# Performance work log

Measured on AMD Instinct MI355X. Metric: run time of the kernel, lower is better.

The kernel has to match this reference:

```python
import jax, jax.numpy as jnp
import numpy as np

DIM = 1024
SEQ_LEN = 4096
K_RANK = 256
HEADS = 16
HEAD_DIM = DIM // HEADS
BATCH = 4


def setup_inputs() -> dict:
    key = jax.random.key(0)
    k1, k2, k3, k4 = jax.random.split(key, 4)
    x = jax.random.normal(k1, (BATCH, SEQ_LEN, DIM), dtype=jnp.float32)
    W_qkv = jax.random.normal(k2, (DIM, 3 * DIM), dtype=jnp.float32) * (DIM ** -0.5)
    E = jax.random.normal(k3, (SEQ_LEN, K_RANK), dtype=jnp.float32)
    W_out = jax.random.normal(k4, (DIM, DIM), dtype=jnp.float32) * (DIM ** -0.5)
    b_out = jnp.zeros((DIM,), dtype=jnp.float32)
    return {"x": x, "W_qkv": W_qkv, "E": E, "W_out": W_out, "b_out": b_out}


def reference(x, W_qkv, E, W_out, b_out):
    B, N, D = x.shape
    scale = HEAD_DIM ** -0.5
    qkv = x @ W_qkv                                    # [B, N, 3D]
    q, k, v = jnp.split(qkv, 3, axis=-1)
    # [B, N, D] -> [B, H, N, hd]
    reshape_heads = lambda t: t.reshape(B, N, HEADS, HEAD_DIM).transpose(0, 2, 1, 3)
    q, k, v = map(reshape_heads, (q, k, v))
    # Linformer low-rank projection along sequence: [B, H, N, hd] -> [B, H, k, hd]
    k_proj = jnp.einsum('bhnd,nk->bhkd', k, E)
    v_proj = jnp.einsum('bhnd,nk->bhkd', v, E)
    scores = jnp.einsum('bhnd,bhkd->bhnk', q, k_proj) * scale  # [B, H, N, k]
    attn = jax.nn.softmax(scores, axis=-1)
    out = jnp.einsum('bhnk,bhkd->bhnd', attn, v_proj)  # [B, H, N, hd]
    out = out.transpose(0, 2, 1, 3).reshape(B, N, D)
    return out @ W_out + b_out
```

## Files before the change

kernel.cpp:

```cpp
#include <hip/hip_runtime.h>
#include <hip/hip_bf16.h>

typedef _Float16 f16;
typedef __attribute__((ext_vector_type(4))) _Float16 f16x4;
typedef __attribute__((ext_vector_type(8))) _Float16 f16x8;
typedef __attribute__((ext_vector_type(4))) float f32x4;

#define DIM 1024
#define SEQ 4096
#define KRNK 256
#define NH 16
#define HD 64
#define NB 4
#define ROWS (NB*SEQ)
#define NSPLIT 4

typedef const void __attribute__((address_space(1))) as1cv;
typedef void __attribute__((address_space(3))) as3v;

static __device__ __forceinline__ void glds16(const void* g, void* l) {
  __builtin_amdgcn_global_load_lds((as1cv*)g, (as3v*)l, 16, 0, 0);
}

__global__ __launch_bounds__(256) void k_prep_w_all(const float* __restrict__ Wqkv,
                                                    const float* __restrict__ Wout,
                                                    f16* __restrict__ Wph,
                                                    f16* __restrict__ Wpl,
                                                    f16* __restrict__ WoT) {
  __shared__ float tile[64][65];
  int bx = blockIdx.x;
  const float* in; f16* oh; f16* ol; int C; bool split;
  if (bx < 768) { in = Wqkv; oh = Wph; ol = Wpl; C = 3 * DIM; split = true; }
  else { bx -= 768; in = Wout; oh = WoT; ol = nullptr; C = DIM; split = false; }
  const int R = DIM;
  int rtiles = R >> 6;
  int rt = bx % rtiles, ct = bx / rtiles;
  int r0 = rt << 6, c0 = ct << 6, t = threadIdx.x;
#pragma unroll
  for (int i = 0; i < 16; ++i) {
    int e = t + i * 256; int r = e >> 6, c = e & 63;
    tile[r][c] = in[(size_t)(r0 + r) * C + c0 + c];
  }
  __syncthreads();
#pragma unroll
  for (int i = 0; i < 16; ++i) {
    int e = t + i * 256; int c = e >> 6, r = e & 63;
    float v = tile[r][c];
    size_t idx = (size_t)(c0 + c) * R + r0 + r;
    if (split) {
      v *= 256.0f;
      f16 h = (f16)v;
      oh[idx] = h;
      ol[idx] = (f16)(v - (float)h);
    } else {
      oh[idx] = (f16)v;
    }
  }
}

template<bool WH>
__global__ __launch_bounds__(256) void k_tsplit(const float* __restrict__ in,
                                                f16* __restrict__ oh,
                                                f16* __restrict__ oth,
                                                int R, int C) {
  __shared__ __align__(16) f16 tileT[64][66];
  int rtiles = R >> 6;
  int rt = blockIdx.x % rtiles, ct = blockIdx.x / rtiles;
  int r0 = rt << 6, c0 = ct << 6, t = threadIdx.x;
  int cq = (t & 15) * 4, rr = t >> 4;
#pragma unroll
  for (int i = 0; i < 4; ++i) {
    int r = rr + i * 16;
    f32x4 v = *(const f32x4*)&in[(size_t)(r0 + r) * C + c0 + cq];
    f16x4 h4 = {(f16)v[0], (f16)v[1], (f16)v[2], (f16)v[3]};
    if constexpr (WH) *(f16x4*)&oh[(size_t)(r0 + r) * C + c0 + cq] = h4;
#pragma unroll
    for (int k = 0; k < 4; ++k) tileT[cq + k][r] = h4[k];
  }
  __syncthreads();
  {
    int c = t >> 2, seg = t & 3;
    f16x8 a = *(const f16x8*)&tileT[c][seg * 16];
    f16x8 b = *(const f16x8*)&tileT[c][seg * 16 + 8];
    f16* dst = &oth[(size_t)(c0 + c) * R + r0 + seg * 16];
    *(f16x8*)dst = a;
    *(f16x8*)(dst + 8) = b;
  }
}

template<bool ASPL, bool BSPL, int MT, int NT>
static __device__ __forceinline__ void mm_core(
    const f16* __restrict__ Ah, const f16* __restrict__ Al, int lda,
    const f16* __restrict__ Bh, const f16* __restrict__ Bl, int ldb,
    int bm, int bn, int K,
    f16* sAh, f16* sAl, f16* sBh, f16* sBl,
    f32x4 (&acc)[MT / 32][NT / 32]) {
  constexpr int MREP = MT / 32, NREP = NT / 32;
  constexpr int AI = MT / 32, BI = NT / 32;
  const int t = threadIdx.x;
  const int lane = t & 63, w = t >> 6;
  const int wr = w >> 1, wc = w & 1;
  const int l15 = lane & 15, hi = lane >> 4;
  const f32x4 zero = {0.f, 0.f, 0.f, 0.f};
#pragma unroll
  for (int m = 0; m < MREP; ++m)
#pragma unroll
    for (int n = 0; n < NREP; ++n) acc[m][n] = zero;

  for (int kk = 0; kk < K; kk += 64) {
#pragma unroll
    for (int i = 0; i < AI; ++i) {
      int c = t + i * 256;
      int row = c >> 3, cc = c & 7;
      size_t g = (size_t)(bm + row) * lda + kk + ((cc ^ (row & 7)) * 8);
      glds16(Ah + g, &sAh[c * 8]);
      if constexpr (ASPL) glds16(Al + g, &sAl[c * 8]);
    }
#pragma unroll
    for (int i = 0; i < BI; ++i) {
      int c = t + i * 256;
      int row = c >> 3, cc = c & 7;
      size_t g = (size_t)(bn + row) * ldb + kk + ((cc ^ (row & 7)) * 8);
      glds16(Bh + g, &sBh[c * 8]);
      if constexpr (BSPL) glds16(Bl + g, &sBl[c * 8]);
    }
    __syncthreads();

    f16x8 avh[MREP][2], avl[MREP][2], bvh[NREP][2], bvl[NREP][2];
#pragma unroll
    for (int m = 0; m < MREP; ++m)
#pragma unroll
      for (int ks = 0; ks < 2; ++ks) {
        int R = wr * (MT / 2) + m * 16 + l15;
        int off = R * 64 + (((ks * 4 + hi) ^ (R & 7)) * 8);
        avh[m][ks] = *(const f16x8*)&sAh[off];
        if constexpr (ASPL) avl[m][ks] = *(const f16x8*)&sAl[off];
      }
#pragma unroll
    for (int n = 0; n < NREP; ++n)
#pragma unroll
      for (int ks = 0; ks < 2; ++ks) {
        int R = wc * (NT / 2) + n * 16 + l15;
        int off = R * 64 + (((ks * 4 + hi) ^ (R & 7)) * 8);
        bvh[n][ks] = *(const f16x8*)&sBh[off];
        if constexpr (BSPL) bvl[n][ks] = *(const f16x8*)&sBl[off];
      }
#pragma unroll
    for (int m = 0; m < MREP; ++m)
#pragma unroll
      for (int n = 0; n < NREP; ++n)
#pragma unroll
        for (int ks = 0; ks < 2; ++ks) {
          if constexpr (ASPL && BSPL) {
            acc[m][n] = __builtin_amdgcn_mfma_f32_16x16x32_f16(avl[m][ks], bvh[n][ks], acc[m][n], 0, 0, 0);
            acc[m][n] = __builtin_amdgcn_mfma_f32_16x16x32_f16(avh[m][ks], bvl[n][ks], acc[m][n], 0, 0, 0);
          } else if constexpr (BSPL) {
            acc[m][n] = __builtin_amdgcn_mfma_f32_16x16x32_f16(avh[m][ks], bvl[n][ks], acc[m][n], 0, 0, 0);
          }
          acc[m][n] = __builtin_amdgcn_mfma_f32_16x16x32_f16(avh[m][ks], bvh[n][ks], acc[m][n], 0, 0, 0);
        }
    __syncthreads();
  }
}

__global__ __launch_bounds__(256) void k_xe2(const f16* __restrict__ Eth,
                                             const f16* __restrict__ xth,
                                             float* __restrict__ XEp) {
  __shared__ __align__(16) f16 sA[128 * 64];
  __shared__ __align__(16) f16 sB[64 * 64];
  int bx = blockIdx.x;
  int nt = bx & 15, mt = (bx >> 4) & 1, b = (bx >> 5) & 3, sp = bx >> 7;
  int bm = mt << 7, bn = nt << 6;
  int koff = sp * (SEQ / NSPLIT);
  f32x4 acc[4][2];
  mm_core<false, false, 128, 64>(Eth + koff, nullptr, SEQ,
                                 xth + (size_t)b * SEQ + koff, nullptr, ROWS,
                                 bm, bn, SEQ / NSPLIT, sA, nullptr, sB, nullptr, acc);
  const int t = threadIdx.x, lane = t & 63, w = t >> 6;
  const int wr = w >> 1, wc = w & 1, l15 = lane & 15, hi = lane >> 4;
#pragma unroll
  for (int m = 0; m < 4; ++m)
#pragma unroll
    for (int n = 0; n < 2; ++n)
#pragma unroll
      for (int r = 0; r < 4; ++r) {
        int kr = bm + wr * 64 + m * 16 + hi * 4 + r;
        int dd = bn + wc * 32 + n * 16 + l15;
        XEp[(((size_t)sp * NB + b) * KRNK + kr) * DIM + dd] = acc[m][n][r];
      }
}

__global__ __launch_bounds__(256) void k_xered(const float* __restrict__ XEp,
                                               f16* __restrict__ XEh) {
  size_t i = (size_t)blockIdx.x * 256 + threadIdx.x;
  const size_t sstride = (size_t)NB * KRNK * DIM / 4;
  const f32x4* p = (const f32x4*)XEp;
  f32x4 s = p[i];
#pragma unroll
  for (int sp = 1; sp < NSPLIT; ++sp) s += p[i + sp * sstride];
  f16x4 h4 = {(f16)s[0], (f16)s[1], (f16)s[2], (f16)s[3]};
  *(f16x4*)&XEh[i * 4] = h4;
}

__global__ __launch_bounds__(256) void k_gq(const f16* __restrict__ xh,
                                            const f16* __restrict__ Wph,
                                            f16* __restrict__ q) {
  __shared__ __align__(16) f16 sA[128 * 64];
  __shared__ __align__(16) f16 sB[128 * 64];
  int bx = blockIdx.x;
  int mt = bx & 127, nt = bx >> 7;
  int bm = mt << 7, bn = nt << 7;
  f32x4 acc[4][4];
  mm_core<false, false, 128, 128>(xh, nullptr, DIM, Wph, nullptr, DIM, bm, bn, DIM,
                                  sA, nullptr, sB, nullptr, acc);
  const int t = threadIdx.x, lane = t & 63, w = t >> 6;
  const int wr = w >> 1, wc = w & 1, l15 = lane & 15, hi = lane >> 4;
#pragma unroll
  for (int m = 0; m < 4; ++m)
#pragma unroll
    for (int n = 0; n < 4; ++n)
#pragma unroll
      for (int r = 0; r < 4; ++r) {
        int row = bm + wr * 64 + m * 16 + hi * 4 + r;
        int col = bn + wc * 64 + n * 16 + l15;
        q[(size_t)row * DIM + col] = (f16)(acc[m][n][r] * (1.0f / 256.0f));
      }
}

__global__ __launch_bounds__(256) void k_t2(const f16* __restrict__ XEh,
                                            const f16* __restrict__ Wph,
                                            const f16* __restrict__ Wpl,
                                            f16* __restrict__ kph,
                                            f16* __restrict__ vpt) {
  __shared__ __align__(16) f16 sAh[128 * 64];
  __shared__ __align__(16) f16 sBh[64 * 64], sBl[64 * 64];
  int bx = blockIdx.x;
  int nt = bx & 15, mt = (bx >> 4) & 1, b = (bx >> 5) & 3, kv = bx >> 7;
  size_t abase = (size_t)b * KRNK * DIM;
  size_t wbase = (size_t)(DIM + kv * DIM) * DIM;
  f32x4 acc[4][2];
  mm_core<false, true, 128, 64>(XEh + abase, nullptr, DIM, Wph + wbase, Wpl + wbase, DIM,
                                mt << 7, nt << 6, DIM, sAh, nullptr, sBh, sBl, acc);
  const int t = threadIdx.x, lane = t & 63, w = t >> 6;
  const int wr = w >> 1, wc = w & 1, l15 = lane & 15, hi = lane >> 4;
#pragma unroll
  for (int m = 0; m < 4; ++m)
#pragma unroll
    for (int n = 0; n < 2; ++n)
#pragma unroll
      for (int r = 0; r < 4; ++r) {
        int row = (mt << 7) + wr * 64 + m * 16 + hi * 4 + r;
        int col = (nt << 6) + wc * 32 + n * 16 + l15;
        float s = acc[m][n][r] * (1.0f / 256.0f);
        if (!kv) kph[((size_t)(b * KRNK + row)) * DIM + col] = (f16)s;
        else     vpt[((size_t)(b * DIM + col)) * KRNK + row] = (f16)s;
      }
}

__global__ __launch_bounds__(256) void k_attn(const f16* __restrict__ q,
                                              const f16* __restrict__ kph,
                                              const f16* __restrict__ vpt,
                                              f16* __restrict__ oattn) {
  __shared__ __align__(16) f16 sBuf[2][128 * 64];
  __shared__ __align__(16) f16 sP[64 * KRNK];
  int bx0 = blockIdx.x;
  int swz = (bx0 & 7) * 512 + (bx0 >> 3);
  int qb = swz & 63;
  int bh = swz >> 6;
  int b = bh >> 4, h = bh & 15;
  int t = threadIdx.x;
  int lane = t & 63, w = t >> 6;
  int l15 = lane & 15, hi = lane >> 4;

  const f16* kbase = kph + ((size_t)(b * KRNK)) * DIM + h * HD;
  const f16* vbase = vpt + ((size_t)(b * DIM + h * HD)) * KRNK;

  auto stageK = [&](int c, int bufi) {
#pragma unroll
    for (int i = 0; i < 4; ++i) {
      int c2 = t + i * 256;
      int kr = c2 >> 3, sl = c2 & 7;
      glds16(kbase + (size_t)(c * 128 + kr) * DIM + ((sl ^ (kr & 7)) * 8),
             &sBuf[bufi][c2 * 8]);
    }
  };
  auto stageV = [&](int c, int bufi) {
#pragma unroll
    for (int i = 0; i < 4; ++i) {
      int c2 = t + i * 256;
      int hd = c2 >> 4, sl = c2 & 15;
      glds16(vbase + (size_t)hd * KRNK + c * 128 + ((sl ^ (hd & 7)) * 8),
             &sBuf[bufi][c2 * 8]);
    }
  };

  int seqrow = qb * 64 + w * 16 + l15;
  const f16* qg = q + ((size_t)(b * SEQ + seqrow)) * DIM + h * HD;
  f16x8 aq[2];
  aq[0] = *(const f16x8*)(qg + hi * 8);
  aq[1] = *(const f16x8*)(qg + 32 + hi * 8);

  const f32x4 zero = {0.f, 0.f, 0.f, 0.f};
  f32x4 s[16];

  stageK(0, 0);
#pragma unroll
  for (int c = 0; c < 2; ++c) {
    __syncthreads();
    if (c == 0) stageK(1, 1);
    else        stageV(0, 0);
#pragma unroll
    for (int n = 0; n < 8; ++n) {
      int nn = c * 8 + n;
      s[nn] = zero;
      int krl = n * 16 + l15;
#pragma unroll
      for (int ks = 0; ks < 2; ++ks) {
        f16x8 bk = *(const f16x8*)&sBuf[c][krl * 64 + (((ks * 4 + hi) ^ (krl & 7)) * 8)];
        s[nn] = __builtin_amdgcn_mfma_f32_16x16x32_f16(bk, aq[ks], s[nn], 0, 0, 0);
      }
    }
  }

  const float scale = 0.125f;
  float m0 = s[0][0];
#pragma unroll
  for (int n = 0; n < 16; ++n)
#pragma unroll
    for (int r = 0; r < 4; ++r) m0 = fmaxf(m0, s[n][r]);
  m0 = fmaxf(m0, __shfl_xor(m0, 16));
  m0 = fmaxf(m0, __shfl_xor(m0, 32));
  float sm0 = 0.f, sm1 = 0.f, sm2 = 0.f, sm3 = 0.f;
#pragma unroll
  for (int n = 0; n < 16; ++n) {
    float p0 = __expf((s[n][0] - m0) * scale);
    float p1 = __expf((s[n][1] - m0) * scale);
    float p2 = __expf((s[n][2] - m0) * scale);
    float p3 = __expf((s[n][3] - m0) * scale);
    s[n][0] = p0; s[n][1] = p1; s[n][2] = p2; s[n][3] = p3;
    sm0 += p0; sm1 += p1; sm2 += p2; sm3 += p3;
  }
  float sm = (sm0 + sm1) + (sm2 + sm3);
  sm += __shfl_xor(sm, 16);
  sm += __shfl_xor(sm, 32);
  float inv = 1.0f / sm;

  {
    int qrow = w * 16 + l15;
    int qm = qrow & 7;
    f16* rowp = &sP[qrow * KRNK];
#pragma unroll
    for (int n = 0; n < 16; ++n) {
      int chunk = 2 * n + (hi >> 1);
      f16x4 pv = {(f16)s[n][0], (f16)s[n][1], (f16)s[n][2], (f16)s[n][3]};
      *(f16x4*)&rowp[((chunk ^ qm) * 8) + (hi & 1) * 4] = pv;
    }
  }

  f32x4 o[4];
#pragma unroll
  for (int n = 0; n < 4; ++n) o[n] = zero;
  int qloc = w * 16 + l15;
#pragma unroll
  for (int c = 0; c < 2; ++c) {
    __syncthreads();
    if (c == 0) stageV(1, 1);
#pragma unroll
    for (int q4 = 0; q4 < 4; ++q4) {
      int chunk = c * 16 + q4 * 4 + hi;
      f16x8 pa = *(const f16x8*)&sP[qloc * KRNK + ((chunk ^ (qloc & 7)) * 8)];
#pragma unroll
      for (int n = 0; n < 4; ++n) {
        int hd = n * 16 + l15;
        f16x8 bv = *(const f16x8*)&sBuf[c][hd * 128 + (((q4 * 4 + hi) ^ (hd & 7)) * 8)];
        o[n] = __builtin_amdgcn_mfma_f32_16x16x32_f16(pa, bv, o[n], 0, 0, 0);
      }
    }
  }

  float invr[4];
#pragma unroll
  for (int r = 0; r < 4; ++r) invr[r] = __shfl(inv, hi * 4 + r);

  size_t obase = ((size_t)(b * SEQ + qb * 64)) * DIM + h * HD;
#pragma unroll
  for (int n = 0; n < 4; ++n)
#pragma unroll
    for (int r = 0; r < 4; ++r) {
      int qloc2 = w * 16 + hi * 4 + r;
      int hd = n * 16 + l15;
      oattn[obase + (size_t)qloc2 * DIM + hd] = (f16)(o[n][r] * invr[r]);
    }
}

__global__ __launch_bounds__(256) void k_go(const f16* __restrict__ oattn,
                                            const f16* __restrict__ WoT,
                                            const float* __restrict__ bias,
                                            float* __restrict__ out) {
  __shared__ __align__(16) f16 sA[128 * 64];
  __shared__ __align__(16) f16 sB[128 * 64];
  int bx = blockIdx.x;
  int mt = bx & 127, nt = bx >> 7;
  int bm = mt << 7, bn = nt << 7;
  f32x4 acc[4][4];
  mm_core<false, false, 128, 128>(oattn, nullptr, DIM, WoT, nullptr, DIM, bm, bn, DIM,
                                  sA, nullptr, sB, nullptr, acc);
  const int t = threadIdx.x, lane = t & 63, w = t >> 6;
  const int wr = w >> 1, wc = w & 1, l15 = lane & 15, hi = lane >> 4;
#pragma unroll
  for (int m = 0; m < 4; ++m)
#pragma unroll
    for (int n = 0; n < 4; ++n)
#pragma unroll
      for (int r = 0; r < 4; ++r) {
        int row = bm + wr * 64 + m * 16 + hi * 4 + r;
        int col = bn + wc * 64 + n * 16 + l15;
        out[(size_t)row * DIM + col] = acc[m][n][r] + bias[col];
      }
}

extern "C" void kernel_launch(void* const* d_in, const int* in_sizes, int n_in,
                              void* d_out, int out_size, void* d_ws, size_t ws_size,
                              hipStream_t stream) {
  const float* x    = (const float*)d_in[0];
  const float* Wqkv = (const float*)d_in[1];
  const float* E    = (const float*)d_in[2];
  const float* Wout = (const float*)d_in[3];
  const float* bout = (const float*)d_in[4];
  float* out = (float*)d_out;

  char* p = (char*)d_ws;
  f16* Wph = (f16*)p;  p += (size_t)2 * 3 * DIM * DIM;
  f16* Wpl = (f16*)p;  p += (size_t)2 * 3 * DIM * DIM;
  f16* WoT = (f16*)p;  p += (size_t)2 * DIM * DIM;
  f16* xh  = (f16*)p;  p += (size_t)2 * ROWS * DIM;
  f16* xth = (f16*)p;  p += (size_t)2 * DIM * ROWS;
  f16* Eth = (f16*)p;  p += (size_t)2 * KRNK * SEQ;
  f16* XEh = (f16*)p;  p += (size_t)2 * NB * KRNK * DIM;
  f16* kph = (f16*)p;  p += (size_t)2 * NB * KRNK * DIM;
  f16* vpt = (f16*)p;  p += (size_t)2 * NB * DIM * KRNK;
  f16* oattn = (f16*)p; p += (size_t)2 * ROWS * DIM;
  float* XEp = (float*)p;  p += (size_t)4 * NSPLIT * NB * KRNK * DIM;
  size_t need = (size_t)(p - (char*)d_ws);
  if (ws_size < need) return;

  f16* q = xth;

  k_prep_w_all<<<1024, 256, 0, stream>>>(Wqkv, Wout, Wph, Wpl, WoT);
  k_tsplit<true><<<(ROWS / 64) * (DIM / 64), 256, 0, stream>>>(x, xh, xth, ROWS, DIM);
  k_tsplit<false><<<(SEQ / 64) * (KRNK / 64), 256, 0, stream>>>(E, nullptr, Eth, SEQ, KRNK);
  k_xe2<<<512, 256, 0, stream>>>(Eth, xth, XEp);
  k_xered<<<(NB * KRNK * DIM / 4) / 256, 256, 0, stream>>>(XEp, XEh);
  k_gq<<<1024, 256, 0, stream>>>(xh, Wph, q);
  k_t2<<<256, 256, 0, stream>>>(XEh, Wph, Wpl, kph, vpt);
  k_attn<<<64 * 64, 256, 0, stream>>>(q, kph, vpt, oattn);
  k_go<<<1024, 256, 0, stream>>>(oattn, WoT, bout, out);
}
```

Before: 223.8 us.

## Rewrite output projection GEMM as 256x256 double-buffered 8-wave kernel

Replaces the 128x128-tile output projection kernel with a 256x256-tile, 512-thread kernel. It double-buffers LDS, interleaves the async global-to-LDS loads for the next K tile with four MFMA phases of the current tile, and uses XOR-swizzled LDS addressing and setprio around the MFMA bursts. The goal is to raise data reuse and hide global load latency. In exchange it uses 128KB of LDS per block, and the 256-block grid may underfill the 256 CUs or limit occupancy.

```diff
diff --git a/kernel.cpp b/kernel.cpp
--- a/kernel.cpp
+++ b/kernel.cpp
@@ -393,27 +393,106 @@
     }
 }
 
-__global__ __launch_bounds__(256) void k_go(const f16* __restrict__ oattn,
-                                            const f16* __restrict__ WoT,
-                                            const float* __restrict__ bias,
-                                            float* __restrict__ out) {
-  __shared__ __align__(16) f16 sA[128 * 64];
-  __shared__ __align__(16) f16 sB[128 * 64];
-  int bx = blockIdx.x;
-  int mt = bx & 127, nt = bx >> 7;
-  int bm = mt << 7, bn = nt << 7;
-  f32x4 acc[4][4];
-  mm_core<false, false, 128, 128>(oattn, nullptr, DIM, WoT, nullptr, DIM, bm, bn, DIM,
-                                  sA, nullptr, sB, nullptr, acc);
-  const int t = threadIdx.x, lane = t & 63, w = t >> 6;
-  const int wr = w >> 1, wc = w & 1, l15 = lane & 15, hi = lane >> 4;
-#pragma unroll
-  for (int m = 0; m < 4; ++m)
+__global__ __launch_bounds__(512) void k_go8(const f16* __restrict__ oattn,
+                                             const f16* __restrict__ WoT,
+                                             const float* __restrict__ bias,
+                                             float* __restrict__ out) {
+  __shared__ __align__(16) f16 sA[2][256 * 64];
+  __shared__ __align__(16) f16 sB[2][256 * 64];
+  const int bx = blockIdx.x;
+  const int mt = bx & 63, nt = bx >> 6;
+  const int bm = mt << 8, bn = nt << 8;
+  const int t = threadIdx.x;
+  const int lane = t & 63, w = t >> 6;
+  const int wr = w >> 2, wc = w & 3;
+  const int l15 = lane & 15, hi = lane >> 4;
+  const f32x4 zero = {0.f, 0.f, 0.f, 0.f};
+  f32x4 acc[8][4];
+#pragma unroll
+  for (int m = 0; m < 8; ++m)
+#pragma unroll
+    for (int n = 0; n < 4; ++n) acc[m][n] = zero;
+
+  auto stage = [&](const f16* base, int boff, int kk, int half, f16* lds) {
+#pragma unroll
+    for (int i = 0; i < 2; ++i) {
+      int c = t + i * 512;
+      int row = c >> 3, sl = c & 7;
+      glds16(base + (size_t)(boff + half * 128 + row) * DIM + kk + ((sl ^ (row & 7)) * 8),
+             lds + half * 8192 + c * 8);
+    }
+  };
+
+  auto phase = [&](const f16* cA, const f16* cB, int qm, int qn) {
+    f16x8 av[4][2], bv[2][2];
+#pragma unroll
+    for (int mi = 0; mi < 4; ++mi)
+#pragma unroll
+      for (int ks = 0; ks < 2; ++ks) {
+        int R = wr * 128 + (qm * 4 + mi) * 16 + l15;
+        av[mi][ks] = *(const f16x8*)&cA[R * 64 + (((ks * 4 + hi) ^ (R & 7)) * 8)];
+      }
+#pragma unroll
+    for (int ni = 0; ni < 2; ++ni)
+#pragma unroll
+      for (int ks = 0; ks < 2; ++ks) {
+        int R = wc * 64 + (qn * 2 + ni) * 16 + l15;
+        bv[ni][ks] = *(const f16x8*)&cB[R * 64 + (((ks * 4 + hi) ^ (R & 7)) * 8)];
+      }
+    __builtin_amdgcn_s_setprio(1);
+#pragma unroll
+    for (int mi = 0; mi < 4; ++mi)
+#pragma unroll
+      for (int ni = 0; ni < 2; ++ni)
+#pragma unroll
+        for (int ks = 0; ks < 2; ++ks)
+          acc[qm * 4 + mi][qn * 2 + ni] =
+              __builtin_amdgcn_mfma_f32_16x16x32_f16(av[mi][ks], bv[ni][ks],
+                                                     acc[qm * 4 + mi][qn * 2 + ni], 0, 0, 0);
+    __builtin_amdgcn_s_setprio(0);
+  };
+
+  constexpr int NT_K = DIM / 64;
+  stage(oattn, bm, 0, 0, sA[0]);
+  stage(oattn, bm, 0, 1, sA[0]);
+  stage(WoT,   bn, 0, 0, sB[0]);
+  stage(WoT,   bn, 0, 1, sB[0]);
+
+  for (int ti = 0; ti < NT_K; ++ti) {
+    const int cur = ti & 1;
+    const f16* cA = sA[cur];
+    const f16* cB = sB[cur];
+    f16* nA = sA[cur ^ 1];
+    f16* nB = sB[cur ^ 1];
+    const int kk1 = (ti + 1) << 6;
+    const bool pf = (ti + 1 < NT_K);
+    if (pf) {
+      stage(oattn, bm, kk1, 0, nA);
+      asm volatile("s_waitcnt vmcnt(2)" ::: "memory");
+    } else {
+      asm volatile("s_waitcnt vmcnt(0)" ::: "memory");
+    }
+    __builtin_amdgcn_s_barrier();
+    phase(cA, cB, 0, 0);
+    __builtin_amdgcn_s_barrier();
+    if (pf) stage(oattn, bm, kk1, 1, nA);
+    phase(cA, cB, 0, 1);
+    __builtin_amdgcn_s_barrier();
+    if (pf) stage(WoT, bn, kk1, 0, nB);
+    phase(cA, cB, 1, 0);
+    __builtin_amdgcn_s_barrier();
+    if (pf) stage(WoT, bn, kk1, 1, nB);
+    phase(cA, cB, 1, 1);
+    __builtin_amdgcn_s_barrier();
+  }
+
+#pragma unroll
+  for (int m = 0; m < 8; ++m)
 #pragma unroll
     for (int n = 0; n < 4; ++n)
 #pragma unroll
       for (int r = 0; r < 4; ++r) {
-        int row = bm + wr * 64 + m * 16 + hi * 4 + r;
+        int row = bm + wr * 128 + m * 16 + hi * 4 + r;
         int col = bn + wc * 64 + n * 16 + l15;
         out[(size_t)row * DIM + col] = acc[m][n][r] + bias[col];
       }
@@ -454,5 +533,5 @@
   k_gq<<<1024, 256, 0, stream>>>(xh, Wph, q);
   k_t2<<<256, 256, 0, stream>>>(XEh, Wph, Wpl, kph, vpt);
   k_attn<<<64 * 64, 256, 0, stream>>>(q, kph, vpt, oattn);
-  k_go<<<1024, 256, 0, stream>>>(oattn, WoT, bout, out);
-}
+  k_go8<<<256, 512, 0, stream>>>(oattn, WoT, bout, out);
+}
```

New measurement: 230.1 us. +2.8%, slower.
